# Performance work log

Measured on AMD Instinct MI355X. Metric: run time of the kernel, lower is better.

## Reference

```python
import jax, jax.numpy as jnp
import numpy as np

BN_EPS = 1e-5

def setup_inputs() -> dict:
    key = jax.random.key(0)
    k1, k2, k3 = jax.random.split(key, 3)
    B, C, H, W = 8, 96, 56, 56
    Cout = 2 * C  # must equal 2*C for the BatchNorm in the original module
    x = jax.random.normal(k1, (B, C, H, W), dtype=jnp.float32)
    conv_w = jax.random.normal(k2, (Cout, 2 * C), dtype=jnp.float32) * (1.0 / np.sqrt(2 * C))
    conv_b = jax.random.normal(k3, (Cout,), dtype=jnp.float32) * 0.01
    gamma = jnp.ones((Cout,), dtype=jnp.float32)
    beta = jnp.zeros((Cout,), dtype=jnp.float32)
    return {"x": x, "conv_w": conv_w, "conv_b": conv_b, "gamma": gamma, "beta": beta}

def _forward(x, conv_w, conv_b, gamma, beta):
    B, C, H, W = x.shape
    # b c h w -> b n c, n = H*W
    q = x.reshape(B, C, H * W).transpose(0, 2, 1)
    # unscaled self-attention (q == k == v == tokens)
    att = jnp.einsum('bnc,bmc->bnm', q, q)          # [B, N, N]
    att = jax.nn.softmax(att, axis=-1)
    att = jnp.einsum('bnm,bmc->bnc', att, q)        # [B, N, C]
    att = att.transpose(0, 2, 1).reshape(B, C, H, W)
    # max-relative: x_j = max(0, x - att) since x_j starts at zeros
    x_j = jnp.maximum(x - att, 0.0)
    cat = jnp.concatenate([x, x_j], axis=1)          # [B, 2C, H, W]
    # 1x1 conv
    y = jnp.einsum('bchw,oc->bohw', cat, conv_w) + conv_b[None, :, None, None]
    # BatchNorm2d in training mode: biased batch stats over (B, H, W)
    mean = jnp.mean(y, axis=(0, 2, 3), keepdims=True)
    var = jnp.var(y, axis=(0, 2, 3), keepdims=True)
    y = (y - mean) * jax.lax.rsqrt(var + BN_EPS)
    y = y * gamma[None, :, None, None] + beta[None, :, None, None]
    # torch nn.GELU default is exact (erf) GELU
    return jax.nn.gelu(y, approximate=False)

def reference(x, conv_w, conv_b, gamma, beta):
    return _forward(x, conv_w, conv_b, gamma, beta)
```

## Files before the change

### kernel.cpp

```cpp
#include <hip/hip_runtime.h>
#include <hip/hip_bf16.h>

#define B_    8
#define C_    96
#define N_    3136
#define COUT_ 192
#define NTOK_ 25088
#define BN_EPS 1e-5f

#define CROW 200
#define BNC  (B_ * N_ * C_)
#define NSPLIT 3
#define NT98  98

#define K2_V_OFF 6144
#define K2_BUFSZ 14336

typedef __hip_bfloat16 bf16;
typedef unsigned short u16;
typedef unsigned int u32;
typedef __attribute__((ext_vector_type(8))) short short8;
typedef __attribute__((ext_vector_type(16))) float f32x16;

__device__ __forceinline__ u16 f2bf(float f) {
    union { __hip_bfloat16 h; u16 u; } cv;
    cv.h = __float2bfloat16(f);
    return cv.u;
}
__device__ __forceinline__ float bf2f(u16 v) {
    union { u16 u; __hip_bfloat16 h; } cv;
    cv.u = v;
    return __bfloat162float(cv.h);
}
__device__ __forceinline__ u32 packbf2(float lo, float hi) {
    return ((u32)f2bf(hi) << 16) | (u32)f2bf(lo);
}

__device__ __forceinline__ void gload_lds16(const void* g, void* l) {
    __builtin_amdgcn_global_load_lds((const __attribute__((address_space(1))) void*)g,
                                     (__attribute__((address_space(3))) void*)l,
                                     16, 0, 0);
}

__device__ __forceinline__ size_t foff(int t, int kc) {
    return ((size_t)t * 6 + kc) << 9;
}

__global__ __launch_bounds__(256) void transpose_split(const float* __restrict__ x,
                                                       u16* __restrict__ xf_hi,
                                                       u16* __restrict__ xf_lo,
                                                       u16* __restrict__ xc_hi,
                                                       float* __restrict__ norm2) {
    __shared__ float tile[32][33];
    __shared__ float nrm[32];
    const int nb = blockIdx.x * 32;
    const int cb = blockIdx.y * 32;
    const int b  = blockIdx.z;
    const int tid = threadIdx.x;
    const int tx = tid & 31;
    const int ty = tid >> 5;
    if (tid < 32) nrm[tid] = 0.0f;
    float psum = 0.0f;
#pragma unroll
    for (int r = 0; r < 32; r += 8) {
        size_t idx = ((size_t)b * C_ + cb + ty + r) * N_ + nb + tx;
        float v = x[idx];
        tile[ty + r][tx] = v;
        xc_hi[idx] = f2bf(v);
        psum = fmaf(v, v, psum);
    }
    __syncthreads();
    atomicAdd(&nrm[tx], psum);

    {
        const int item  = tid & 127;
        const int is_lo = tid >> 7;
        const int kc_i  = item >> 6;
        const int l     = item & 63;
        const int kcg   = (cb >> 4) + kc_i;
        union { u16 a[8]; short8 v8; } o;
#pragma unroll
        for (int j = 0; j < 8; j++) {
            float v = tile[kc_i * 16 + ((l >> 5) * 8) + j][l & 31];
            u16 h = f2bf(v);
            o.a[j] = is_lo ? f2bf(v - bf2f(h)) : h;
        }
        u16* dst = (is_lo ? xf_lo : xf_hi) +
                   ((size_t)b * NT98 * 6 << 9) + foff(nb >> 5, kcg) + l * 8;
        *(short8*)dst = o.v8;
    }
    __syncthreads();
    if (tid < 32)
        atomicAdd(&norm2[(size_t)b * N_ + nb + tid], nrm[tid]);
}

__global__ __launch_bounds__(256) void cast_w(const float* __restrict__ w,
                                              u16* __restrict__ wf_hi,
                                              u16* __restrict__ wf_lo) {
    int i = blockIdx.x * 256 + threadIdx.x;
    if (i >= COUT_ * 2 * C_) return;
    float v = w[i];
    u16 h  = f2bf(v);
    u16 lo = f2bf(v - bf2f(h));
    int o = i / (2 * C_), c = i % (2 * C_);
    int mt = o >> 5, lrow = o & 31;
    int ks = c >> 4, hi8 = (c >> 3) & 1, j = c & 7;
    size_t d = ((size_t)(mt * 12 + ks) * 64 + hi8 * 32 + lrow) * 8 + j;
    wf_hi[d] = h;
    wf_lo[d] = lo;
}

__global__ __launch_bounds__(256) void norm_max(const float* __restrict__ norm2,
                                                int* __restrict__ maxbits) {
    const int tid = blockIdx.x * 256 + threadIdx.x;
    float m = 0.0f;
    for (int i = tid; i < NTOK_; i += gridDim.x * 256) m = fmaxf(m, norm2[i]);
#pragma unroll
    for (int d = 1; d < 64; d <<= 1) m = fmaxf(m, __shfl_xor(m, d));
    if ((threadIdx.x & 63) == 0) atomicMax(maxbits, __float_as_int(m));
}

__global__ __launch_bounds__(256, 3) void flash_attn_mfma32(const u16* __restrict__ xf_hi,
                                                            const u16* __restrict__ xf_lo,
                                                            const u16* __restrict__ xc_hi,
                                                            const float* __restrict__ norm2,
                                                            const int* __restrict__ maxbits,
                                                            float* __restrict__ attT,
                                                            float* __restrict__ l_arr) {
    __shared__ __align__(16) char LDSU[2][K2_BUFSZ];
    const int b     = blockIdx.y;
    const int i0    = blockIdx.x * 128;
    const int split = blockIdx.z;
    const int kt0   = (NT98 * split) / NSPLIT;
    const int kt1   = (NT98 * (split + 1)) / NSPLIT;
    const int tid   = threadIdx.x;
    const int lane  = tid & 63;
    const int w     = tid >> 6;
    const int col   = lane & 31;
    const int g     = lane >> 5;

    const u16* fh = xf_hi + ((size_t)b * NT98 * 6 << 9);
    const u16* fl = xf_lo + ((size_t)b * NT98 * 6 << 9);
    const u16* vh = xc_hi + (size_t)b * C_ * N_;

    u32 loff[4], dofs[4];
#pragma unroll
    for (int j = 0; j < 4; j++) {
        int s = w + 4 * j;
        if (s >= 14) { loff[j] = 0; dofs[j] = 0; continue; }
        if (s < 6) {
            loff[j] = (u32)(s * 1024 + lane * 16);
            dofs[j] = (u32)(s * 1024);
        } else {
            int t = s - 6;
            int p = t * 64 + lane;
            int ch = p / 5, c = p % 5;
            if (c > 3) c = 3;
            loff[j] = (ch < 96) ? (u32)(ch * (N_ * 2) + c * 16) : 0u;
            dofs[j] = (u32)(K2_V_OFF + t * 1024);
        }
    }

    int qt = blockIdx.x * 4 + w;
    if (qt > NT98 - 1) qt = NT98 - 1;
    const int qrow  = i0 + w * 32 + col;
    const int qrowc = qrow < N_ ? qrow : N_ - 1;
    short8 qh[6], ql[6];
#pragma unroll
    for (int kc = 0; kc < 6; kc++) {
        qh[kc] = *(const short8*)&fh[foff(qt, kc) + lane * 8];
        ql[kc] = *(const short8*)&fl[foff(qt, kc) + lane * 8];
    }
    const float maxn2 = __int_as_float(*maxbits);
    const float m_i   = sqrtf(norm2[(size_t)b * N_ + qrowc] * maxn2);
    float l_acc = 0.0f;
    f32x16 O0 = {0}, O1 = {0}, O2 = {0};

    auto stage = [&](int nbuf, int kt) {
        const u32 ktK = (u32)kt * 6144u;
        const u32 ktV = (u32)kt * 64u;
#pragma unroll
        for (int j = 0; j < 4; j++) {
            int s = w + 4 * j;
            if (s >= 14) break;
            const char* sb = (s < 6) ? (const char*)fh + ktK
                                     : (const char*)vh + ktV;
            gload_lds16(sb + loff[j], (char*)&LDSU[nbuf][0] + dofs[j]);
        }
    };

    stage(0, kt0);
    __syncthreads();

    const int g16 = g * 16;
    int buf = 0;
    for (int kt = kt0; kt < kt1; kt++) {
        if (kt + 1 < kt1) stage(buf ^ 1, kt + 1);

        const char* Lb = (const char*)&LDSU[buf][0];

        short8 kl[6];
#pragma unroll
        for (int kc = 0; kc < 6; kc++)
            kl[kc] = *(const short8*)&fl[foff(kt, kc) + lane * 8];

        f32x16 S = {0};
        __builtin_amdgcn_s_setprio(1);
#pragma unroll
        for (int kc = 0; kc < 6; kc++) {
            short8 kh = *(const short8*)(Lb + kc * 1024 + lane * 16);
            S = __builtin_amdgcn_mfma_f32_32x32x16_bf16(kh, ql[kc], S, 0, 0, 0);
            S = __builtin_amdgcn_mfma_f32_32x32x16_bf16(kl[kc], qh[kc], S, 0, 0, 0);
            S = __builtin_amdgcn_mfma_f32_32x32x16_bf16(kh, qh[kc], S, 0, 0, 0);
        }
        __builtin_amdgcn_s_setprio(0);

        float p[16];
#pragma unroll
        for (int r = 0; r < 16; r++) {
            p[r] = __expf(S[r] - m_i);
            l_acc += p[r];
        }
        u32 w8[8];
#pragma unroll
        for (int q = 0; q < 8; q++) w8[q] = packbf2(p[2 * q], p[2 * q + 1]);

        __builtin_amdgcn_s_setprio(1);
#pragma unroll
        for (int kc = 0; kc < 2; kc++) {
            const int qb = kc * 4;
            u32 a0 = w8[qb + 0], a1 = w8[qb + 1];
            u32 a2 = w8[qb + 2], a3 = w8[qb + 3];
            u32 s0 = __shfl_xor((int)a0, 32), s1 = __shfl_xor((int)a1, 32);
            u32 s2 = __shfl_xor((int)a2, 32), s3 = __shfl_xor((int)a3, 32);
            union { short8 v; u32 u[4]; } Bf;
            Bf.u[0] = g ? s2 : a0;
            Bf.u[1] = g ? s3 : a1;
            Bf.u[2] = g ? a2 : s0;
            Bf.u[3] = g ? a3 : s1;
            const int vo = K2_V_OFF + col * 80 + kc * 32 + g16;
            short8 v0 = *(const short8*)(Lb + vo);
            short8 v1 = *(const short8*)(Lb + vo + 2560);
            short8 v2 = *(const short8*)(Lb + vo + 5120);
            O0 = __builtin_amdgcn_mfma_f32_32x32x16_bf16(v0, Bf.v, O0, 0, 0, 0);
            O1 = __builtin_amdgcn_mfma_f32_32x32x16_bf16(v1, Bf.v, O1, 0, 0, 0);
            O2 = __builtin_amdgcn_mfma_f32_32x32x16_bf16(v2, Bf.v, O2, 0, 0, 0);
        }
        __builtin_amdgcn_s_setprio(0);

        __syncthreads();
        buf ^= 1;
    }

    if (qrow < N_) {
        float* ab = attT + (size_t)b * C_ * N_ + qrow;
#pragma unroll
        for (int r = 0; r < 16; r++) {
            int c = (r & 3) + 8 * (r >> 2) + 4 * g;
            atomicAdd(&ab[(size_t)(c)      * N_], O0[r]);
            atomicAdd(&ab[(size_t)(c + 32) * N_], O1[r]);
            atomicAdd(&ab[(size_t)(c + 64) * N_], O2[r]);
        }
        float l_tot = l_acc + __shfl_xor(l_acc, 32);
        if (g == 0) atomicAdd(&l_arr[(size_t)b * N_ + qrow], l_tot);
    }
}

__global__ __launch_bounds__(128, 3) void conv_mfma(const float* __restrict__ x,
                                                    const float* __restrict__ attT,
                                                    const float* __restrict__ l_arr,
                                                    const u16* __restrict__ wf_hi,
                                                    const u16* __restrict__ wf_lo,
                                                    const float* __restrict__ convb,
                                                    float* __restrict__ y) {
    __shared__ u16 ch[32 * CROW];
    __shared__ u16 cl[32 * CROW];
    __shared__ float invl[32];
    const int b   = blockIdx.x / (N_ / 32);
    const int n0  = (blockIdx.x % (N_ / 32)) * 32;
    const int tid = threadIdx.x;

    if (tid < 32) invl[tid] = 1.0f / l_arr[(size_t)b * N_ + n0 + tid];
    __syncthreads();

    const float* xb = x    + (size_t)b * C_ * N_ + n0;
    const float* ab = attT + (size_t)b * C_ * N_ + n0;
    for (int e = tid; e < 32 * C_; e += 128) {
        int c = e >> 5, t = e & 31;
        float xv = xb[(size_t)c * N_ + t];
        float au = ab[(size_t)c * N_ + t];
        float xj = fmaxf(xv - au * invl[t], 0.0f);
        u16 h1 = f2bf(xv);
        ch[t * CROW + c] = h1;
        cl[t * CROW + c] = f2bf(xv - bf2f(h1));
        u16 h2 = f2bf(xj);
        ch[t * CROW + C_ + c] = h2;
        cl[t * CROW + C_ + c] = f2bf(xj - bf2f(h2));
    }
    __syncthreads();

    const int lane = tid & 63;
    const int w    = tid >> 6;
    const int col  = lane & 31;
    const int g    = lane >> 5;
    const int m0   = w * 3;

    f32x16 A[3] = {{0}, {0}, {0}};
#pragma unroll
    for (int ks = 0; ks < 12; ks++) {
        const int k0 = ks * 16;
        short8 bh = *(const short8*)&ch[col * CROW + k0 + g * 8];
        short8 bl = *(const short8*)&cl[col * CROW + k0 + g * 8];
#pragma unroll
        for (int mt = 0; mt < 3; mt++) {
            const size_t wo = (size_t)((m0 + mt) * 12 + ks) * 512 + lane * 8;
            short8 ah = *(const short8*)&wf_hi[wo];
            short8 al = *(const short8*)&wf_lo[wo];
            A[mt] = __builtin_amdgcn_mfma_f32_32x32x16_bf16(ah, bl, A[mt], 0, 0, 0);
            A[mt] = __builtin_amdgcn_mfma_f32_32x32x16_bf16(al, bh, A[mt], 0, 0, 0);
            A[mt] = __builtin_amdgcn_mfma_f32_32x32x16_bf16(ah, bh, A[mt], 0, 0, 0);
        }
    }

    float* yb = y + (size_t)b * COUT_ * N_ + n0 + col;
#pragma unroll
    for (int mt = 0; mt < 3; mt++)
#pragma unroll
        for (int r = 0; r < 16; r++) {
            int o = (m0 + mt) * 32 + (r & 3) + 8 * (r >> 2) + 4 * g;
            yb[(size_t)o * N_] = A[mt][r] + convb[o];
        }
}

__global__ __launch_bounds__(256) void bn_partial(const float* __restrict__ y,
                                                  float* __restrict__ pb) {
    const int o   = blockIdx.x;
    const int b   = blockIdx.y;
    const int tid = threadIdx.x;
    float s = 0.0f, q = 0.0f;
    const float4* p = (const float4*)(y + (size_t)(b * COUT_ + o) * N_);
    for (int i = tid; i < N_ / 4; i += 256) {
        float4 v = p[i];
        s += v.x + v.y + v.z + v.w;
        q += v.x * v.x + v.y * v.y + v.z * v.z + v.w * v.w;
    }
#pragma unroll
    for (int d = 1; d < 64; d <<= 1) {
        s += __shfl_xor(s, d);
        q += __shfl_xor(q, d);
    }
    __shared__ float wss[4], wqq[4];
    if ((tid & 63) == 0) { wss[tid >> 6] = s; wqq[tid >> 6] = q; }
    __syncthreads();
    if (tid == 0) {
        pb[b * COUT_ + o]                = wss[0] + wss[1] + wss[2] + wss[3];
        pb[B_ * COUT_ + b * COUT_ + o]   = wqq[0] + wqq[1] + wqq[2] + wqq[3];
    }
}

__global__ __launch_bounds__(192) void bn_finish(const float* __restrict__ pb,
                                                 const float* __restrict__ gamma,
                                                 const float* __restrict__ beta,
                                                 float* __restrict__ ss) {
    const int o = threadIdx.x;
    float s = 0.0f, q = 0.0f;
#pragma unroll
    for (int b = 0; b < B_; b++) {
        s += pb[b * COUT_ + o];
        q += pb[B_ * COUT_ + b * COUT_ + o];
    }
    const float invn = 1.0f / (float)NTOK_;
    float mean = s * invn;
    float var  = q * invn - mean * mean;
    float sc   = gamma[o] * rsqrtf(var + BN_EPS);
    ss[o]         = sc;
    ss[COUT_ + o] = beta[o] - mean * sc;
}

__global__ __launch_bounds__(256) void bn_gelu_out(const float* __restrict__ y,
                                                   const float* __restrict__ ss,
                                                   float* __restrict__ out) {
    const int total4 = (B_ * COUT_ * N_) / 4;
    int i = blockIdx.x * 256 + threadIdx.x;
    if (i >= total4) return;
    int base = i * 4;
    int o = (base / N_) % COUT_;
    float sc = ss[o], sh = ss[COUT_ + o];
    float4 v = *(const float4*)&y[base];
    float u0 = fmaf(v.x, sc, sh), u1 = fmaf(v.y, sc, sh);
    float u2 = fmaf(v.z, sc, sh), u3 = fmaf(v.w, sc, sh);
    const float k = 0.70710678118654752f;
    float4 g;
    g.x = 0.5f * u0 * (1.0f + erff(u0 * k));
    g.y = 0.5f * u1 * (1.0f + erff(u1 * k));
    g.z = 0.5f * u2 * (1.0f + erff(u2 * k));
    g.w = 0.5f * u3 * (1.0f + erff(u3 * k));
    *(float4*)&out[base] = g;
}

extern "C" void kernel_launch(void* const* d_in, const int* in_sizes, int n_in,
                              void* d_out, int out_size, void* d_ws, size_t ws_size,
                              hipStream_t stream) {
    const float* x     = (const float*)d_in[0];
    const float* w     = (const float*)d_in[1];
    const float* cb    = (const float*)d_in[2];
    const float* gamma = (const float*)d_in[3];
    const float* beta  = (const float*)d_in[4];

    u16* xf_hi = (u16*)d_ws;
    u16* xf_lo = xf_hi + (size_t)BNC;
    u16* xc_hi = xf_lo + (size_t)BNC;
    float* attT  = (float*)(xc_hi + (size_t)BNC);
    u16* wf_hi = (u16*)(attT + (size_t)BNC);
    u16* wf_lo = wf_hi + COUT_ * 2 * C_;
    float* y     = (float*)(wf_lo + COUT_ * 2 * C_);
    float* ss    = y + (size_t)B_ * COUT_ * N_;
    float* l_arr = ss + 2 * COUT_;
    float* norm2 = l_arr + NTOK_;
    int*   maxb  = (int*)(norm2 + NTOK_);
    float* pb    = attT;

    hipMemsetAsync(l_arr, 0, NTOK_ * sizeof(float), stream);
    hipMemsetAsync(norm2, 0, NTOK_ * sizeof(float), stream);
    hipMemsetAsync(maxb, 0, sizeof(int), stream);
    hipMemsetAsync(attT, 0, (size_t)BNC * sizeof(float), stream);

    transpose_split<<<dim3(N_ / 32, C_ / 32, B_), 256, 0, stream>>>(x, xf_hi, xf_lo, xc_hi, norm2);
    cast_w<<<dim3((COUT_ * 2 * C_ + 255) / 256), 256, 0, stream>>>(w, wf_hi, wf_lo);
    norm_max<<<dim3(25), 256, 0, stream>>>(norm2, maxb);
    flash_attn_mfma32<<<dim3((N_ + 127) / 128, B_, NSPLIT), 256, 0, stream>>>(
        xf_hi, xf_lo, xc_hi, norm2, maxb, attT, l_arr);
    conv_mfma<<<dim3(B_ * (N_ / 32)), 128, 0, stream>>>(x, attT, l_arr, wf_hi, wf_lo, cb, y);
    bn_partial<<<dim3(COUT_, B_), 256, 0, stream>>>(y, pb);
    bn_finish<<<dim3(1), 192, 0, stream>>>(pb, gamma, beta, ss);
    bn_gelu_out<<<dim3((B_ * COUT_ * N_ / 4 + 255) / 256), 256, 0, stream>>>(y, ss, (float*)d_out);
}
```

Before: 206.7 us.

## Fuse BatchNorm partial statistics into conv epilogue and merge memsets

The conv kernel now reduces per-block sums and sums of squares across lanes with shuffles and writes them to a partials buffer. This removes the separate bn_partial pass that reread the whole conv output. bn_finish is parallelised per output channel to reduce those partials. The transpose kernel also writes xc_hi as packed bf16 pairs from shared memory instead of scalar stores, and three small memsets are merged into one. The cost is extra shuffle work and serialized partial writes in the conv epilogue.

```diff
diff --git a/kernel.cpp b/kernel.cpp
--- a/kernel.cpp
+++ b/kernel.cpp
@@ -12,6 +12,7 @@
 #define BNC  (B_ * N_ * C_)
 #define NSPLIT 3
 #define NT98  98
+#define NCONVB (B_ * (N_ / 32))
 
 #define K2_V_OFF 6144
 #define K2_BUFSZ 14336
@@ -66,11 +67,24 @@
         size_t idx = ((size_t)b * C_ + cb + ty + r) * N_ + nb + tx;
         float v = x[idx];
         tile[ty + r][tx] = v;
-        xc_hi[idx] = f2bf(v);
         psum = fmaf(v, v, psum);
     }
     __syncthreads();
     atomicAdd(&nrm[tx], psum);
+
+#pragma unroll
+    for (int it = 0; it < 2; it++) {
+        int e  = tid + it * 256;
+        int cc = e >> 4;
+        int np = e & 15;
+        u32 pv = packbf2(0.0f, 0.0f);
+        {
+            float v0 = tile[cc][2 * np];
+            float v1 = tile[cc][2 * np + 1];
+            pv = ((u32)f2bf(v1) << 16) | (u32)f2bf(v0);
+        }
+        *(u32*)&xc_hi[((size_t)b * C_ + cb + cc) * N_ + nb + 2 * np] = pv;
+    }
 
     {
         const int item  = tid & 127;
@@ -272,7 +286,8 @@
                                                     const u16* __restrict__ wf_hi,
                                                     const u16* __restrict__ wf_lo,
                                                     const float* __restrict__ convb,
-                                                    float* __restrict__ y) {
+                                                    float* __restrict__ y,
+                                                    float* __restrict__ pbs) {
     __shared__ u16 ch[32 * CROW];
     __shared__ u16 cl[32 * CROW];
     __shared__ float invl[32];
@@ -328,21 +343,31 @@
 #pragma unroll
         for (int r = 0; r < 16; r++) {
             int o = (m0 + mt) * 32 + (r & 3) + 8 * (r >> 2) + 4 * g;
-            yb[(size_t)o * N_] = A[mt][r] + convb[o];
-        }
-}
-
-__global__ __launch_bounds__(256) void bn_partial(const float* __restrict__ y,
-                                                  float* __restrict__ pb) {
+            float v = A[mt][r] + convb[o];
+            yb[(size_t)o * N_] = v;
+            float s = v, q = v * v;
+#pragma unroll
+            for (int d = 1; d < 32; d <<= 1) {
+                s += __shfl_xor(s, d);
+                q += __shfl_xor(q, d);
+            }
+            if (col == 0) {
+                pbs[(size_t)o * NCONVB + blockIdx.x] = s;
+                pbs[(size_t)COUT_ * NCONVB + (size_t)o * NCONVB + blockIdx.x] = q;
+            }
+        }
+}
+
+__global__ __launch_bounds__(256) void bn_finish(const float* __restrict__ pbs,
+                                                 const float* __restrict__ gamma,
+                                                 const float* __restrict__ beta,
+                                                 float* __restrict__ ss) {
     const int o   = blockIdx.x;
-    const int b   = blockIdx.y;
     const int tid = threadIdx.x;
     float s = 0.0f, q = 0.0f;
-    const float4* p = (const float4*)(y + (size_t)(b * COUT_ + o) * N_);
-    for (int i = tid; i < N_ / 4; i += 256) {
-        float4 v = p[i];
-        s += v.x + v.y + v.z + v.w;
-        q += v.x * v.x + v.y * v.y + v.z * v.z + v.w * v.w;
+    for (int i = tid; i < NCONVB; i += 256) {
+        s += pbs[(size_t)o * NCONVB + i];
+        q += pbs[(size_t)COUT_ * NCONVB + (size_t)o * NCONVB + i];
     }
 #pragma unroll
     for (int d = 1; d < 64; d <<= 1) {
@@ -353,28 +378,15 @@
     if ((tid & 63) == 0) { wss[tid >> 6] = s; wqq[tid >> 6] = q; }
     __syncthreads();
     if (tid == 0) {
-        pb[b * COUT_ + o]                = wss[0] + wss[1] + wss[2] + wss[3];
-        pb[B_ * COUT_ + b * COUT_ + o]   = wqq[0] + wqq[1] + wqq[2] + wqq[3];
-    }
-}
-
-__global__ __launch_bounds__(192) void bn_finish(const float* __restrict__ pb,
-                                                 const float* __restrict__ gamma,
-                                                 const float* __restrict__ beta,
-                                                 float* __restrict__ ss) {
-    const int o = threadIdx.x;
-    float s = 0.0f, q = 0.0f;
-#pragma unroll
-    for (int b = 0; b < B_; b++) {
-        s += pb[b * COUT_ + o];
-        q += pb[B_ * COUT_ + b * COUT_ + o];
-    }
-    const float invn = 1.0f / (float)NTOK_;
-    float mean = s * invn;
-    float var  = q * invn - mean * mean;
-    float sc   = gamma[o] * rsqrtf(var + BN_EPS);
-    ss[o]         = sc;
-    ss[COUT_ + o] = beta[o] - mean * sc;
+        float st = wss[0] + wss[1] + wss[2] + wss[3];
+        float qt = wqq[0] + wqq[1] + wqq[2] + wqq[3];
+        const float invn = 1.0f / (float)NTOK_;
+        float mean = st * invn;
+        float var  = qt * invn - mean * mean;
+        float sc   = gamma[o] * rsqrtf(var + BN_EPS);
+        ss[o]         = sc;
+        ss[COUT_ + o] = beta[o] - mean * sc;
+    }
 }
 
 __global__ __launch_bounds__(256) void bn_gelu_out(const float* __restrict__ y,
@@ -418,11 +430,9 @@
     float* l_arr = ss + 2 * COUT_;
     float* norm2 = l_arr + NTOK_;
     int*   maxb  = (int*)(norm2 + NTOK_);
-    float* pb    = attT;
-
-    hipMemsetAsync(l_arr, 0, NTOK_ * sizeof(float), stream);
-    hipMemsetAsync(norm2, 0, NTOK_ * sizeof(float), stream);
-    hipMemsetAsync(maxb, 0, sizeof(int), stream);
+    float* pbs   = (float*)(maxb + 1);
+
+    hipMemsetAsync(l_arr, 0, (2 * NTOK_) * sizeof(float) + sizeof(int), stream);
     hipMemsetAsync(attT, 0, (size_t)BNC * sizeof(float), stream);
 
     transpose_split<<<dim3(N_ / 32, C_ / 32, B_), 256, 0, stream>>>(x, xf_hi, xf_lo, xc_hi, norm2);
@@ -430,8 +440,7 @@
     norm_max<<<dim3(25), 256, 0, stream>>>(norm2, maxb);
     flash_attn_mfma32<<<dim3((N_ + 127) / 128, B_, NSPLIT), 256, 0, stream>>>(
         xf_hi, xf_lo, xc_hi, norm2, maxb, attT, l_arr);
-    conv_mfma<<<dim3(B_ * (N_ / 32)), 128, 0, stream>>>(x, attT, l_arr, wf_hi, wf_lo, cb, y);
-    bn_partial<<<dim3(COUT_, B_), 256, 0, stream>>>(y, pb);
-    bn_finish<<<dim3(1), 192, 0, stream>>>(pb, gamma, beta, ss);
+    conv_mfma<<<dim3(NCONVB), 128, 0, stream>>>(x, attT, l_arr, wf_hi, wf_lo, cb, y, pbs);
+    bn_finish<<<dim3(COUT_), 256, 0, stream>>>(pbs, gamma, beta, ss);
     bn_gelu_out<<<dim3((B_ * COUT_ * N_ / 4 + 255) / 256), 256, 0, stream>>>(y, ss, (float*)d_out);
 }
```

Result: slower. 215.0 us (+4.0%).
